# Kernel tuning notes

Hardware: AMD Instinct MI355X
Metric: run time of the kernel (lower is better)

The kernel has to match this reference:

```python
import jax, jax.numpy as jnp
import numpy as np
import math

B, S = 32, 2048
D_MODEL, D_STATE = 1024, 256
DT_MIN, DT_MAX = 1e-3, 0.1
LN_EPS = 1e-5


def setup_inputs() -> dict:
    key = jax.random.key(0)
    k_x, k_b, k_c = jax.random.split(key, 3)
    x = jax.random.normal(k_x, (B, S, D_MODEL), dtype=jnp.float32)
    log_lambda_real = jnp.linspace(math.log(DT_MIN), math.log(DT_MAX), D_STATE).astype(jnp.float32)
    log_b = jax.random.uniform(k_b, (D_STATE, 1), minval=-0.5, maxval=0.5, dtype=jnp.float32)
    c = jax.random.normal(k_c, (1, D_STATE), dtype=jnp.float32) / math.sqrt(D_STATE)
    log_d = jnp.zeros((1,), jnp.float32)
    log_step = jnp.asarray(math.log(DT_MIN), jnp.float32)
    alpha = jnp.asarray(0.7, jnp.float32)
    ln_gamma = jnp.ones((D_STATE,), jnp.float32)
    ln_beta = jnp.zeros((D_STATE,), jnp.float32)
    return {
        "x": x,
        "log_lambda_real": log_lambda_real,
        "log_b": log_b,
        "c": c,
        "log_d": log_d,
        "log_step": log_step,
        "alpha": alpha,
        "ln_gamma": ln_gamma,
        "ln_beta": ln_beta,
    }


def _layer_norm(h, gamma, beta):
    mu = jnp.mean(h, axis=-1, keepdims=True)
    var = jnp.mean((h - mu) ** 2, axis=-1, keepdims=True)
    return (h - mu) * jax.lax.rsqrt(var + LN_EPS) * gamma + beta


def reference(x, log_lambda_real, log_b, c, log_d, log_step, alpha, ln_gamma, ln_beta):
    lam = -jnp.exp(log_lambda_real)          # [N]
    b = jnp.exp(log_b)[:, 0]                 # [N]
    d = jnp.exp(log_d)                       # [1]
    step = jnp.exp(log_step)                 # scalar
    # bilinear discretization
    a_disc = (2.0 + step * lam) / (2.0 - step * lam)        # [N]
    b_disc = step * (1.0 + a_disc) * b / 2.0                 # [N]

    u = jnp.mean(x, axis=-1)                 # [B, S] per-timestep scalar drive
    c_row = c[0]                             # [N]

    def scan_step(h, u_t):
        # h: [B, N], u_t: [B]
        h = a_disc[None, :] * h + b_disc[None, :] * u_t[:, None]
        h = _layer_norm(h, ln_gamma, ln_beta)
        s = h @ c_row                        # [B]
        return h, s

    h0 = jnp.zeros((x.shape[0], a_disc.shape[0]), x.dtype)
    _, s = jax.lax.scan(scan_step, h0, u.T)  # s: [S, B]
    y = s.T[:, :, None] + d * x              # [B, S, D] (broadcast of scalar readout)
    a_sig = jax.nn.sigmoid(alpha)
    return a_sig * x + (1.0 - a_sig) * y
```

## Files before the change

kernel.cpp:

```cpp
#include <hip/hip_runtime.h>

constexpr int B = 32, S = 2048, D = 1024, N = 256;
constexpr int NCHUNK = 32;
constexpr int SBLK   = 32;
constexpr int WBLK   = 128;

#define DEV __device__ __forceinline__

template <int CTRL>
DEV float dpp_add(float x) {
  int y = __builtin_amdgcn_update_dpp(0, __float_as_int(x), CTRL, 0xF, 0xF, true);
  return x + __int_as_float(y);
}

DEV float rdlane(float v, int l) {
  return __int_as_float(__builtin_amdgcn_readlane(__float_as_int(v), l));
}

DEV void wave_reduce3(float& a, float& b, float& c) {
  a = dpp_add<0x111>(a); b = dpp_add<0x111>(b); c = dpp_add<0x111>(c);
  a = dpp_add<0x112>(a); b = dpp_add<0x112>(b); c = dpp_add<0x112>(c);
  a = dpp_add<0x114>(a); b = dpp_add<0x114>(b); c = dpp_add<0x114>(c);
  a = dpp_add<0x118>(a); b = dpp_add<0x118>(b); c = dpp_add<0x118>(c);
  a = dpp_add<0x142>(a); b = dpp_add<0x142>(b); c = dpp_add<0x142>(c);
  a = dpp_add<0x143>(a); b = dpp_add<0x143>(b); c = dpp_add<0x143>(c);
  a = rdlane(a, 63);
  b = rdlane(b, 63);
  c = rdlane(c, 63);
}

DEV float ld_agent(const float* p) {
  return __hip_atomic_load(p, __ATOMIC_RELAXED, __HIP_MEMORY_SCOPE_AGENT);
}
DEV int ld_flag(const int* p) {
  return __hip_atomic_load(p, __ATOMIC_RELAXED, __HIP_MEMORY_SCOPE_AGENT);
}

__global__ __launch_bounds__(1024) void fused(
    const float4* __restrict__ x4, const float* __restrict__ llr,
    const float* __restrict__ logb, const float* __restrict__ c,
    const float* __restrict__ lstep, const float* __restrict__ gma,
    const float* __restrict__ bta, const float* __restrict__ logd,
    const float* __restrict__ alpha, float* __restrict__ u,
    float* __restrict__ s, int* __restrict__ uflag, int* __restrict__ sflag,
    float4* __restrict__ o4) {
  const int wv   = threadIdx.x >> 6;
  const int lane = threadIdx.x & 63;

  if (blockIdx.x >= SBLK) {
    const int wb = blockIdx.x - SBLK;
    const int b  = wb >> 2;
    const int i  = ((wb & 3) << 4) | wv;

    for (int ch = 0; ch < NCHUNK; ++ch) {
      const int t = (ch << 6) | i;
      const float4* xr = x4 + (size_t)(b * S + t) * (D / 4);
      float sm = 0.f;
#pragma unroll
      for (int k = 0; k < 4; ++k) {
        float4 v = xr[lane + (k << 6)];
        sm += (v.x + v.y) + (v.z + v.w);
      }
#pragma unroll
      for (int off = 32; off; off >>= 1) sm += __shfl_xor(sm, off, 64);
      if (lane == 0) atomicExch(&u[b * S + t], sm * (1.f / 1024.f));
      if ((ch & 7) == 7) {
        asm volatile("s_waitcnt vmcnt(0)" ::: "memory");
        __syncthreads();
        if (threadIdx.x == 0) atomicAdd(&uflag[(b << 5) + (ch >> 3)], 1);
      }
    }

    const float asig = 1.f / (1.f + expf(-alpha[0]));
    const float dd   = expf(logd[0]);
    const float cx   = asig + (1.f - asig) * dd;
    const float cs   = 1.f - asig;
    for (int ch = 0; ch < NCHUNK; ++ch) {
      if (threadIdx.x == 0) {
        while (ld_flag(&sflag[b << 5]) < ch + 1) __builtin_amdgcn_s_sleep(8);
      }
      __syncthreads();
      const int t = (ch << 6) | i;
      const float sv = cs * ld_agent(&s[b * S + t]);
      const float4* xr   = x4 + (size_t)(b * S + t) * (D / 4);
      float4*       orow = o4 + (size_t)(b * S + t) * (D / 4);
#pragma unroll
      for (int k = 0; k < 4; ++k) {
        float4 v = xr[lane + (k << 6)];
        float4 o;
        o.x = fmaf(cx, v.x, sv);
        o.y = fmaf(cx, v.y, sv);
        o.z = fmaf(cx, v.z, sv);
        o.w = fmaf(cx, v.w, sv);
        orow[lane + (k << 6)] = o;
      }
    }
  } else if (wv == 0) {
    const int b = blockIdx.x;
    __builtin_amdgcn_s_setprio(1);
    const float stp = expf(lstep[0]);

    float ag[4], ab[4], bd[4], cg[4];
    float Gp = 0.f, BCp = 0.f, d0 = 0.f;
#pragma unroll
    for (int k = 0; k < 4; ++k) {
      const int n = (k << 6) | lane;
      const float lam = -expf(llr[n]);
      const float sl  = stp * lam;
      const float adisc = (2.f + sl) / (2.f - sl);
      const float bdisc = stp * (1.f + adisc) * expf(logb[n]) * 0.5f;
      const float g  = gma[n];
      const float be = bta[n];
      const float cc = c[n];
      ag[k] = adisc * g;
      ab[k] = adisc * be;
      bd[k] = bdisc;
      cg[k] = cc * g;
      Gp  += cg[k];
      BCp += cc * be;
    }
    wave_reduce3(Gp, BCp, d0);
    const float G = Gp, BC = BCp;
    const float Ceps = 65536.f * 1e-5f;

    const float* urow = u + b * S;
    float* srow = s + b * S;

    while (ld_flag(&uflag[b << 5]) < 4) __builtin_amdgcn_s_sleep(2);
    __threadfence();
    float uch = ld_agent(urow + lane);
    const float u0 = rdlane(uch, 0);
    float z0 = bd[0] * u0, z1 = bd[1] * u0, z2 = bd[2] * u0, z3 = bd[3] * u0;

    for (int chn = 0; chn < NCHUNK; ++chn) {
      float uch_next = uch;
      if (chn < NCHUNK - 1) {
        if (((chn + 1) & 7) == 0) {
          while (ld_flag(&uflag[(b << 5) + ((chn + 1) >> 3)]) < 4)
            __builtin_amdgcn_s_sleep(2);
          __threadfence();
        }
        uch_next = ld_agent(urow + ((chn + 1) << 6) + lane);
      }
      float stk = 0.f;
#pragma unroll
      for (int tt = 0; tt < 64; ++tt) {
        float s1 = (z0 + z1) + (z2 + z3);
        float s2 = fmaf(z0, z0, z1 * z1) + fmaf(z2, z2, z3 * z3);
        float s3 = fmaf(z0, cg[0], z1 * cg[1]) + fmaf(z2, cg[2], z3 * cg[3]);
        wave_reduce3(s1, s2, s3);
        const float q = fmaf(256.f, s2, fmaf(-s1, s1, Ceps));
        const float r = __builtin_amdgcn_rsqf(q);
        const float st = fmaf(r, fmaf(256.f, s3, -s1 * G), BC);
        stk = (lane == tt) ? st : stk;

        const float un = (tt < 63) ? rdlane(uch, tt + 1) : rdlane(uch_next, 0);
        const float w0 = fmaf(256.f, z0, -s1);
        const float w1 = fmaf(256.f, z1, -s1);
        const float w2 = fmaf(256.f, z2, -s1);
        const float w3 = fmaf(256.f, z3, -s1);
        z0 = fmaf(ag[0] * w0, r, fmaf(bd[0], un, ab[0]));
        z1 = fmaf(ag[1] * w1, r, fmaf(bd[1], un, ab[1]));
        z2 = fmaf(ag[2] * w2, r, fmaf(bd[2], un, ab[2]));
        z3 = fmaf(ag[3] * w3, r, fmaf(bd[3], un, ab[3]));
      }
      asm volatile("s_waitcnt vmcnt(0)" ::: "memory");
      if (lane == 0) atomicExch(&sflag[b << 5], chn);
      atomicExch(&srow[(chn << 6) + lane], stk);
      uch = uch_next;
    }
    asm volatile("s_waitcnt vmcnt(0)" ::: "memory");
    if (lane == 0) atomicExch(&sflag[b << 5], NCHUNK);
  }
}

extern "C" void kernel_launch(void* const* d_in, const int* in_sizes, int n_in,
                              void* d_out, int out_size, void* d_ws, size_t ws_size,
                              hipStream_t stream) {
  const float* x     = (const float*)d_in[0];
  const float* llr   = (const float*)d_in[1];
  const float* logb  = (const float*)d_in[2];
  const float* c     = (const float*)d_in[3];
  const float* logd  = (const float*)d_in[4];
  const float* lstep = (const float*)d_in[5];
  const float* alpha = (const float*)d_in[6];
  const float* gma   = (const float*)d_in[7];
  const float* bta   = (const float*)d_in[8];

  float* u     = (float*)d_ws;
  float* s     = u + B * S;
  int*   uflag = (int*)(s + B * S);
  int*   sflag = uflag + B * 32;

  hipMemsetAsync(uflag, 0, 2 * B * 32 * sizeof(int), stream);
  fused<<<SBLK + WBLK, 1024, 0, stream>>>(
      (const float4*)x, llr, logb, c, lstep, gma, bta, logd, alpha,
      u, s, uflag, sflag, (float4*)d_out);
}
```

Before: 599.6 us.

## Interleave two batch scans per wave to hide reduction latency

Each scan wave now carries two independent batch recurrences (A and B) and reduces all six sums in one interleaved DPP chain, so the latency of one batch's reduction overlaps with the other's. This halves the number of scan blocks, and the inner loop unroll drops from full to 8. Each time step doubles its per-wave ALU work, which lengthens the serial critical path if the DPP chain was not latency-bound, and the partial unroll may add loop overhead.

```diff
diff --git a/kernel.cpp b/kernel.cpp
--- a/kernel.cpp
+++ b/kernel.cpp
@@ -2,7 +2,7 @@
 
 constexpr int B = 32, S = 2048, D = 1024, N = 256;
 constexpr int NCHUNK = 32;
-constexpr int SBLK   = 32;
+constexpr int SBLK   = 16;
 constexpr int WBLK   = 128;
 
 #define DEV __device__ __forceinline__
@@ -29,6 +29,24 @@
   c = rdlane(c, 63);
 }
 
+DEV void wave_reduce6(float& a, float& b, float& c, float& d, float& e,
+                      float& f) {
+  a = dpp_add<0x111>(a); b = dpp_add<0x111>(b); c = dpp_add<0x111>(c);
+  d = dpp_add<0x111>(d); e = dpp_add<0x111>(e); f = dpp_add<0x111>(f);
+  a = dpp_add<0x112>(a); b = dpp_add<0x112>(b); c = dpp_add<0x112>(c);
+  d = dpp_add<0x112>(d); e = dpp_add<0x112>(e); f = dpp_add<0x112>(f);
+  a = dpp_add<0x114>(a); b = dpp_add<0x114>(b); c = dpp_add<0x114>(c);
+  d = dpp_add<0x114>(d); e = dpp_add<0x114>(e); f = dpp_add<0x114>(f);
+  a = dpp_add<0x118>(a); b = dpp_add<0x118>(b); c = dpp_add<0x118>(c);
+  d = dpp_add<0x118>(d); e = dpp_add<0x118>(e); f = dpp_add<0x118>(f);
+  a = dpp_add<0x142>(a); b = dpp_add<0x142>(b); c = dpp_add<0x142>(c);
+  d = dpp_add<0x142>(d); e = dpp_add<0x142>(e); f = dpp_add<0x142>(f);
+  a = dpp_add<0x143>(a); b = dpp_add<0x143>(b); c = dpp_add<0x143>(c);
+  d = dpp_add<0x143>(d); e = dpp_add<0x143>(e); f = dpp_add<0x143>(f);
+  a = rdlane(a, 63); b = rdlane(b, 63); c = rdlane(c, 63);
+  d = rdlane(d, 63); e = rdlane(e, 63); f = rdlane(f, 63);
+}
+
 DEV float ld_agent(const float* p) {
   return __hip_atomic_load(p, __ATOMIC_RELAXED, __HIP_MEMORY_SCOPE_AGENT);
 }
@@ -96,7 +114,7 @@
       }
     }
   } else if (wv == 0) {
-    const int b = blockIdx.x;
+    const int b0 = blockIdx.x << 1;
     __builtin_amdgcn_s_setprio(1);
     const float stp = expf(lstep[0]);
 
@@ -123,54 +141,90 @@
     const float G = Gp, BC = BCp;
     const float Ceps = 65536.f * 1e-5f;
 
-    const float* urow = u + b * S;
-    float* srow = s + b * S;
-
-    while (ld_flag(&uflag[b << 5]) < 4) __builtin_amdgcn_s_sleep(2);
+    const float* urowA = u + b0 * S;
+    const float* urowB = u + (b0 + 1) * S;
+    float* srowA = s + b0 * S;
+    float* srowB = s + (b0 + 1) * S;
+
+    while (ld_flag(&uflag[b0 << 5]) < 4 ||
+           ld_flag(&uflag[(b0 + 1) << 5]) < 4)
+      __builtin_amdgcn_s_sleep(2);
     __threadfence();
-    float uch = ld_agent(urow + lane);
-    const float u0 = rdlane(uch, 0);
-    float z0 = bd[0] * u0, z1 = bd[1] * u0, z2 = bd[2] * u0, z3 = bd[3] * u0;
+    float uchA = ld_agent(urowA + lane);
+    float uchB = ld_agent(urowB + lane);
+    const float u0A = rdlane(uchA, 0);
+    const float u0B = rdlane(uchB, 0);
+    float zA0 = bd[0] * u0A, zA1 = bd[1] * u0A, zA2 = bd[2] * u0A,
+          zA3 = bd[3] * u0A;
+    float zB0 = bd[0] * u0B, zB1 = bd[1] * u0B, zB2 = bd[2] * u0B,
+          zB3 = bd[3] * u0B;
 
     for (int chn = 0; chn < NCHUNK; ++chn) {
-      float uch_next = uch;
+      float uchA_next = uchA, uchB_next = uchB;
       if (chn < NCHUNK - 1) {
         if (((chn + 1) & 7) == 0) {
-          while (ld_flag(&uflag[(b << 5) + ((chn + 1) >> 3)]) < 4)
+          const int q = (chn + 1) >> 3;
+          while (ld_flag(&uflag[(b0 << 5) + q]) < 4 ||
+                 ld_flag(&uflag[((b0 + 1) << 5) + q]) < 4)
             __builtin_amdgcn_s_sleep(2);
           __threadfence();
         }
-        uch_next = ld_agent(urow + ((chn + 1) << 6) + lane);
-      }
-      float stk = 0.f;
-#pragma unroll
+        uchA_next = ld_agent(urowA + ((chn + 1) << 6) + lane);
+        uchB_next = ld_agent(urowB + ((chn + 1) << 6) + lane);
+      }
+      float stkA = 0.f, stkB = 0.f;
+#pragma unroll 8
       for (int tt = 0; tt < 64; ++tt) {
-        float s1 = (z0 + z1) + (z2 + z3);
-        float s2 = fmaf(z0, z0, z1 * z1) + fmaf(z2, z2, z3 * z3);
-        float s3 = fmaf(z0, cg[0], z1 * cg[1]) + fmaf(z2, cg[2], z3 * cg[3]);
-        wave_reduce3(s1, s2, s3);
-        const float q = fmaf(256.f, s2, fmaf(-s1, s1, Ceps));
-        const float r = __builtin_amdgcn_rsqf(q);
-        const float st = fmaf(r, fmaf(256.f, s3, -s1 * G), BC);
-        stk = (lane == tt) ? st : stk;
-
-        const float un = (tt < 63) ? rdlane(uch, tt + 1) : rdlane(uch_next, 0);
-        const float w0 = fmaf(256.f, z0, -s1);
-        const float w1 = fmaf(256.f, z1, -s1);
-        const float w2 = fmaf(256.f, z2, -s1);
-        const float w3 = fmaf(256.f, z3, -s1);
-        z0 = fmaf(ag[0] * w0, r, fmaf(bd[0], un, ab[0]));
-        z1 = fmaf(ag[1] * w1, r, fmaf(bd[1], un, ab[1]));
-        z2 = fmaf(ag[2] * w2, r, fmaf(bd[2], un, ab[2]));
-        z3 = fmaf(ag[3] * w3, r, fmaf(bd[3], un, ab[3]));
+        float s1A = (zA0 + zA1) + (zA2 + zA3);
+        float s2A = fmaf(zA0, zA0, zA1 * zA1) + fmaf(zA2, zA2, zA3 * zA3);
+        float s3A = fmaf(zA0, cg[0], zA1 * cg[1]) + fmaf(zA2, cg[2], zA3 * cg[3]);
+        float s1B = (zB0 + zB1) + (zB2 + zB3);
+        float s2B = fmaf(zB0, zB0, zB1 * zB1) + fmaf(zB2, zB2, zB3 * zB3);
+        float s3B = fmaf(zB0, cg[0], zB1 * cg[1]) + fmaf(zB2, cg[2], zB3 * cg[3]);
+        wave_reduce6(s1A, s2A, s3A, s1B, s2B, s3B);
+        const float qA = fmaf(256.f, s2A, fmaf(-s1A, s1A, Ceps));
+        const float qB = fmaf(256.f, s2B, fmaf(-s1B, s1B, Ceps));
+        const float rA = __builtin_amdgcn_rsqf(qA);
+        const float rB = __builtin_amdgcn_rsqf(qB);
+        const float stA = fmaf(rA, fmaf(256.f, s3A, -s1A * G), BC);
+        const float stB = fmaf(rB, fmaf(256.f, s3B, -s1B * G), BC);
+        stkA = (lane == tt) ? stA : stkA;
+        stkB = (lane == tt) ? stB : stkB;
+
+        float unA, unB;
+        if (tt != 63) {
+          unA = rdlane(uchA, tt + 1);
+          unB = rdlane(uchB, tt + 1);
+        } else {
+          unA = rdlane(uchA_next, 0);
+          unB = rdlane(uchB_next, 0);
+        }
+        const float wA0 = fmaf(256.f, zA0, -s1A);
+        const float wA1 = fmaf(256.f, zA1, -s1A);
+        const float wA2 = fmaf(256.f, zA2, -s1A);
+        const float wA3 = fmaf(256.f, zA3, -s1A);
+        const float wB0 = fmaf(256.f, zB0, -s1B);
+        const float wB1 = fmaf(256.f, zB1, -s1B);
+        const float wB2 = fmaf(256.f, zB2, -s1B);
+        const float wB3 = fmaf(256.f, zB3, -s1B);
+        zA0 = fmaf(ag[0] * wA0, rA, fmaf(bd[0], unA, ab[0]));
+        zA1 = fmaf(ag[1] * wA1, rA, fmaf(bd[1], unA, ab[1]));
+        zA2 = fmaf(ag[2] * wA2, rA, fmaf(bd[2], unA, ab[2]));
+        zA3 = fmaf(ag[3] * wA3, rA, fmaf(bd[3], unA, ab[3]));
+        zB0 = fmaf(ag[0] * wB0, rB, fmaf(bd[0], unB, ab[0]));
+        zB1 = fmaf(ag[1] * wB1, rB, fmaf(bd[1], unB, ab[1]));
+        zB2 = fmaf(ag[2] * wB2, rB, fmaf(bd[2], unB, ab[2]));
+        zB3 = fmaf(ag[3] * wB3, rB, fmaf(bd[3], unB, ab[3]));
       }
       asm volatile("s_waitcnt vmcnt(0)" ::: "memory");
-      if (lane == 0) atomicExch(&sflag[b << 5], chn);
-      atomicExch(&srow[(chn << 6) + lane], stk);
-      uch = uch_next;
+      if (lane < 2) atomicExch(&sflag[(b0 + lane) << 5], chn);
+      atomicExch(&srowA[(chn << 6) + lane], stkA);
+      atomicExch(&srowB[(chn << 6) + lane], stkB);
+      uchA = uchA_next;
+      uchB = uchB_next;
     }
     asm volatile("s_waitcnt vmcnt(0)" ::: "memory");
-    if (lane == 0) atomicExch(&sflag[b << 5], NCHUNK);
+    if (lane < 2) atomicExch(&sflag[(b0 + lane) << 5], NCHUNK);
   }
 }
 
```

Measured after the change: 900.3 us. +50.1%, slower.

## Precompute next-step reduction sums algebraically to move the wave reduction off the rsqrt path

Applied to the files above, without the earlier changes.

Rewrites the scan recurrence so the three per-step sums (sum z, sum z^2, sum c*g*z) are built from four reductions of the pre-scale term v, plus constant sums over bd and ab precomputed at setup. Because P1, P2, P3 and P6 depend only on v and k, the DPP reduction no longer waits on r. This shortens the serial dependency chain of each timestep. It also lowers loop unroll to 16 and adds a min-blocks hint to launch bounds. The expanded sum-of-squares form may lose floating-point accuracy through cancellation.

```diff
diff --git a/kernel.cpp b/kernel.cpp
--- a/kernel.cpp
+++ b/kernel.cpp
@@ -29,6 +29,16 @@
   c = rdlane(c, 63);
 }
 
+DEV void wave_reduce4(float& a, float& b, float& c, float& d) {
+  a = dpp_add<0x111>(a); b = dpp_add<0x111>(b); c = dpp_add<0x111>(c); d = dpp_add<0x111>(d);
+  a = dpp_add<0x112>(a); b = dpp_add<0x112>(b); c = dpp_add<0x112>(c); d = dpp_add<0x112>(d);
+  a = dpp_add<0x114>(a); b = dpp_add<0x114>(b); c = dpp_add<0x114>(c); d = dpp_add<0x114>(d);
+  a = dpp_add<0x118>(a); b = dpp_add<0x118>(b); c = dpp_add<0x118>(c); d = dpp_add<0x118>(d);
+  a = dpp_add<0x142>(a); b = dpp_add<0x142>(b); c = dpp_add<0x142>(c); d = dpp_add<0x142>(d);
+  a = dpp_add<0x143>(a); b = dpp_add<0x143>(b); c = dpp_add<0x143>(c); d = dpp_add<0x143>(d);
+  a = rdlane(a, 63); b = rdlane(b, 63); c = rdlane(c, 63); d = rdlane(d, 63);
+}
+
 DEV float ld_agent(const float* p) {
   return __hip_atomic_load(p, __ATOMIC_RELAXED, __HIP_MEMORY_SCOPE_AGENT);
 }
@@ -36,7 +46,7 @@
   return __hip_atomic_load(p, __ATOMIC_RELAXED, __HIP_MEMORY_SCOPE_AGENT);
 }
 
-__global__ __launch_bounds__(1024) void fused(
+__global__ __launch_bounds__(1024, 4) void fused(
     const float4* __restrict__ x4, const float* __restrict__ llr,
     const float* __restrict__ logb, const float* __restrict__ c,
     const float* __restrict__ lstep, const float* __restrict__ gma,
@@ -101,7 +111,9 @@
     const float stp = expf(lstep[0]);
 
     float ag[4], ab[4], bd[4], cg[4];
-    float Gp = 0.f, BCp = 0.f, d0 = 0.f;
+    float Gp = 0.f, BCp = 0.f, SBDp = 0.f;
+    float SABp = 0.f, SBD2p = 0.f, SBDABp = 0.f;
+    float SAB2p = 0.f, SCBDp = 0.f, SCABp = 0.f;
 #pragma unroll
     for (int k = 0; k < 4; ++k) {
       const int n = (k << 6) | lane;
@@ -116,11 +128,22 @@
       ab[k] = adisc * be;
       bd[k] = bdisc;
       cg[k] = cc * g;
-      Gp  += cg[k];
-      BCp += cc * be;
-    }
-    wave_reduce3(Gp, BCp, d0);
+      Gp    += cg[k];
+      BCp   += cc * be;
+      SBDp  += bd[k];
+      SABp  += ab[k];
+      SBD2p += bd[k] * bd[k];
+      SBDABp+= bd[k] * ab[k];
+      SAB2p += ab[k] * ab[k];
+      SCBDp += cg[k] * bd[k];
+      SCABp += cg[k] * ab[k];
+    }
+    wave_reduce3(Gp, BCp, SBDp);
+    wave_reduce3(SABp, SBD2p, SBDABp);
+    wave_reduce3(SAB2p, SCBDp, SCABp);
     const float G = Gp, BC = BCp;
+    const float SBD = SBDp, SAB = SABp, SBD2 = SBD2p;
+    const float SBDAB = SBDABp, SAB2 = SAB2p, SCBD = SCBDp, SCAB = SCABp;
     const float Ceps = 65536.f * 1e-5f;
 
     const float* urow = u + b * S;
@@ -131,6 +154,9 @@
     float uch = ld_agent(urow + lane);
     const float u0 = rdlane(uch, 0);
     float z0 = bd[0] * u0, z1 = bd[1] * u0, z2 = bd[2] * u0, z3 = bd[3] * u0;
+    float s1 = u0 * SBD;
+    float s2 = u0 * u0 * SBD2;
+    float s3 = u0 * SCBD;
 
     for (int chn = 0; chn < NCHUNK; ++chn) {
       float uch_next = uch;
@@ -143,26 +169,42 @@
         uch_next = ld_agent(urow + ((chn + 1) << 6) + lane);
       }
       float stk = 0.f;
-#pragma unroll
+#pragma unroll 16
       for (int tt = 0; tt < 64; ++tt) {
-        float s1 = (z0 + z1) + (z2 + z3);
-        float s2 = fmaf(z0, z0, z1 * z1) + fmaf(z2, z2, z3 * z3);
-        float s3 = fmaf(z0, cg[0], z1 * cg[1]) + fmaf(z2, cg[2], z3 * cg[3]);
-        wave_reduce3(s1, s2, s3);
-        const float q = fmaf(256.f, s2, fmaf(-s1, s1, Ceps));
-        const float r = __builtin_amdgcn_rsqf(q);
+        const float q  = fmaf(256.f, s2, fmaf(-s1, s1, Ceps));
+        const float r  = __builtin_amdgcn_rsqf(q);
         const float st = fmaf(r, fmaf(256.f, s3, -s1 * G), BC);
         stk = (lane == tt) ? st : stk;
 
-        const float un = (tt < 63) ? rdlane(uch, tt + 1) : rdlane(uch_next, 0);
+        float un;
+        if (tt != 63) un = rdlane(uch, tt + 1);
+        else          un = rdlane(uch_next, 0);
+
         const float w0 = fmaf(256.f, z0, -s1);
         const float w1 = fmaf(256.f, z1, -s1);
         const float w2 = fmaf(256.f, z2, -s1);
         const float w3 = fmaf(256.f, z3, -s1);
-        z0 = fmaf(ag[0] * w0, r, fmaf(bd[0], un, ab[0]));
-        z1 = fmaf(ag[1] * w1, r, fmaf(bd[1], un, ab[1]));
-        z2 = fmaf(ag[2] * w2, r, fmaf(bd[2], un, ab[2]));
-        z3 = fmaf(ag[3] * w3, r, fmaf(bd[3], un, ab[3]));
+        const float v0 = ag[0] * w0, v1 = ag[1] * w1;
+        const float v2 = ag[2] * w2, v3 = ag[3] * w3;
+        const float k0 = fmaf(bd[0], un, ab[0]);
+        const float k1 = fmaf(bd[1], un, ab[1]);
+        const float k2 = fmaf(bd[2], un, ab[2]);
+        const float k3 = fmaf(bd[3], un, ab[3]);
+        z0 = fmaf(v0, r, k0);
+        z1 = fmaf(v1, r, k1);
+        z2 = fmaf(v2, r, k2);
+        z3 = fmaf(v3, r, k3);
+        float P1 = (v0 + v1) + (v2 + v3);
+        float P2 = fmaf(v0, v0, v1 * v1) + fmaf(v2, v2, v3 * v3);
+        float P3 = fmaf(v0, k0, v1 * k1) + fmaf(v2, k2, v3 * k3);
+        float P6 = fmaf(v0, cg[0], v1 * cg[1]) + fmaf(v2, cg[2], v3 * cg[3]);
+        wave_reduce4(P1, P2, P3, P6);
+        const float Sk1 = fmaf(un, SBD, SAB);
+        const float Sk2 = fmaf(un, fmaf(un, SBD2, 2.f * SBDAB), SAB2);
+        const float Sck = fmaf(un, SCBD, SCAB);
+        s1 = fmaf(r, P1, Sk1);
+        s2 = fmaf(r, fmaf(r, P2, 2.f * P3), Sk2);
+        s3 = fmaf(r, P6, Sck);
       }
       asm volatile("s_waitcnt vmcnt(0)" ::: "memory");
       if (lane == 0) atomicExch(&sflag[b << 5], chn);
```

After: 765.1 us. 27.6% more time.
